# Optimization experiments

Hardware: AMD Instinct MI355X
Metric: run time of the kernel (lower is better)

The kernel has to match this reference:

```python
import jax, jax.numpy as jnp
import numpy as np

N = 100000
E = 1600000
NFEAT = 256
NHIDDEN = 128
NCLASS = 40
NLAYERS = 8
INIT_T = 0.5


def setup_inputs() -> dict:
    key = jax.random.key(0)
    ks = jax.random.split(key, 9)
    x = jax.random.normal(ks[0], (N, NFEAT), dtype=jnp.float32)
    edge_row = jax.random.randint(ks[1], (E,), 0, N, dtype=jnp.int32)
    edge_col = jax.random.randint(ks[2], (E,), 0, N, dtype=jnp.int32)
    # small weights so the Chebyshev recurrence stays numerically tame
    edge_weight = jax.random.uniform(ks[3], (E,), dtype=jnp.float32) * (2.0 / 16.0)
    b1 = 1.0 / np.sqrt(NFEAT)
    fc1_w = jax.random.uniform(ks[4], (NFEAT, NHIDDEN), minval=-b1, maxval=b1, dtype=jnp.float32)
    fc1_b = jax.random.uniform(ks[5], (NHIDDEN,), minval=-b1, maxval=b1, dtype=jnp.float32)
    b2 = 1.0 / np.sqrt(NHIDDEN)
    fc2_w = jax.random.uniform(ks[6], (NHIDDEN, NCLASS), minval=-b2, maxval=b2, dtype=jnp.float32)
    fc2_b = jax.random.uniform(ks[7], (NCLASS,), minval=-b2, maxval=b2, dtype=jnp.float32)
    thetas = jnp.full((NLAYERS,), INIT_T, dtype=jnp.float32)
    return {"x": x, "edge_row": edge_row, "edge_col": edge_col,
            "edge_weight": edge_weight, "fc1_w": fc1_w, "fc1_b": fc1_b,
            "fc2_w": fc2_w, "fc2_b": fc2_b, "thetas": thetas}


def _spmm(edge_row, edge_col, edge_weight, t):
    # out[r] = sum_{e: row[e]=r} w[e] * t[col[e]]   (sparse L @ T)
    msgs = edge_weight[:, None] * t[edge_col]  # [E, H]
    return jax.ops.segment_sum(msgs, edge_row, num_segments=N)


def reference(x, edge_row, edge_col, edge_weight, fc1_w, fc1_b, fc2_w, fc2_b, thetas):
    # eval mode: dropout is identity
    h = jax.nn.relu(x @ fc1_w + fc1_b)  # [N, H]
    # filter 0: T_0 = h, poly = theta_0 * T_0
    t0 = h
    poly = thetas[0] * t0
    # filter 1: T_1 = L @ T_0
    t1 = _spmm(edge_row, edge_col, edge_weight, t0)
    poly = poly + thetas[1] * t1
    # remaining filters, replicating the original prevs-update order exactly
    prev0, prev1 = t0, t1
    for i in range(2, NLAYERS):
        ti = 2.0 * _spmm(edge_row, edge_col, edge_weight, prev0) - prev1
        prev1 = prev0
        prev0 = ti
        poly = poly + thetas[i] * ti
    y = poly @ fc2_w + fc2_b  # [N, nclass]
    return jax.nn.log_softmax(y, axis=1)
```

## Files before the change

kernel.cpp:

```cpp
#include <hip/hip_runtime.h>
#include <hip/hip_bf16.h>


#define NFEAT 256
#define NHID  128
#define NCLS  40
#define ELLS  48

typedef __hip_bfloat16 bf16;
typedef __attribute__((ext_vector_type(8))) short bf16x8;
typedef __attribute__((ext_vector_type(4))) float f32x4;

__device__ inline float2 load2b(const bf16* p) {
    __hip_bfloat162 v = *(const __hip_bfloat162*)p;
    return make_float2(__bfloat162float(v.x), __bfloat162float(v.y));
}
__device__ inline void store2b(bf16* p, float2 v) {
    __hip_bfloat162 o;
    o.x = __float2bfloat16(v.x);
    o.y = __float2bfloat16(v.y);
    *(__hip_bfloat162*)p = o;
}

__global__ void zero_ints(int* __restrict__ p, int n) {
    int i = blockIdx.x * blockDim.x + threadIdx.x;
    if (i < n) p[i] = 0;
}

__global__ void scatter_ell(const int* __restrict__ erow, const int* __restrict__ ecol,
                            const float* __restrict__ ew, int* __restrict__ deg,
                            int2* __restrict__ cw, int E) {
    int e = blockIdx.x * blockDim.x + threadIdx.x;
    if (e < E) {
        int r = erow[e];
        int p = atomicAdd(&deg[r], 1);
        if (p < ELLS)
            cw[(size_t)r * ELLS + p] = make_int2(ecol[e], __float_as_int(ew[e]));
    }
}

__global__ void hist_kernel(const int* __restrict__ erow, int* __restrict__ deg, int E) {
    int e = blockIdx.x * blockDim.x + threadIdx.x;
    if (e < E) atomicAdd(&deg[erow[e]], 1);
}

__global__ void assign_starts(const int* __restrict__ deg, int* __restrict__ counter,
                              int* __restrict__ row_start, int* __restrict__ cursor, int N) {
    int r = blockIdx.x * blockDim.x + threadIdx.x;
    int lane = threadIdx.x & 63;
    int d = (r < N) ? deg[r] : 0;
    int x = d;
    #pragma unroll
    for (int off = 1; off < 64; off <<= 1) {
        int y = __shfl_up(x, off);
        if (lane >= off) x += y;
    }
    int base = 0;
    if (lane == 63) base = atomicAdd(counter, x);
    base = __shfl(base, 63);
    int start = base + (x - d);
    if (r < N) {
        row_start[r] = start;
        cursor[r] = start;
    }
}

__global__ void scatter_compact(const int* __restrict__ erow, const int* __restrict__ ecol,
                                const float* __restrict__ ew, int* __restrict__ cursor,
                                int2* __restrict__ cw, int E) {
    int e = blockIdx.x * blockDim.x + threadIdx.x;
    if (e < E) {
        int r = erow[e];
        int p = atomicAdd(&cursor[r], 1);
        cw[p] = make_int2(ecol[e], __float_as_int(ew[e]));
    }
}

__global__ __launch_bounds__(256) void fc1_mfma(
    const float* __restrict__ x, const float* __restrict__ W,
    const float* __restrict__ bias, bf16* __restrict__ t0, int n) {
    __shared__ __align__(16) bf16 As[128 * 40];
    __shared__ __align__(16) bf16 Bs[128 * 40];

    const int tid = threadIdx.x;
    const int wave = tid >> 6;
    const int lane = tid & 63;
    const int quad = lane >> 4;
    const int lm = lane & 15;
    const int block_row = blockIdx.x * 128;

    f32x4 acc[2][8];
    #pragma unroll
    for (int s = 0; s < 2; ++s)
        #pragma unroll
        for (int t = 0; t < 8; ++t)
            acc[s][t] = (f32x4){0.f, 0.f, 0.f, 0.f};

    float bcol[8];
    #pragma unroll
    for (int t = 0; t < 8; ++t) bcol[t] = bias[t * 16 + lm];

    for (int kc = 0; kc < NFEAT; kc += 32) {
        #pragma unroll
        for (int i = 0; i < 4; ++i) {
            int idx = tid + 256 * i;
            int row = idx >> 3;
            int c4 = idx & 7;
            int grow = block_row + row;
            float4 v = make_float4(0.f, 0.f, 0.f, 0.f);
            if (grow < n) v = *(const float4*)&x[(size_t)grow * NFEAT + kc + c4 * 4];
            __hip_bfloat162 lo2, hi2;
            lo2.x = __float2bfloat16(v.x); lo2.y = __float2bfloat16(v.y);
            hi2.x = __float2bfloat16(v.z); hi2.y = __float2bfloat16(v.w);
            *(__hip_bfloat162*)&As[row * 40 + c4 * 4] = lo2;
            *(__hip_bfloat162*)&As[row * 40 + c4 * 4 + 2] = hi2;
        }
        #pragma unroll
        for (int i = 0; i < 4; ++i) {
            int idx = tid + 256 * i;
            int nn = idx & 127;
            int k4 = idx >> 7;
            const float* wp = &W[(size_t)(kc + k4 * 4) * NHID + nn];
            float v0 = wp[0];
            float v1 = wp[NHID];
            float v2 = wp[2 * NHID];
            float v3 = wp[3 * NHID];
            __hip_bfloat162 lo2, hi2;
            lo2.x = __float2bfloat16(v0); lo2.y = __float2bfloat16(v1);
            hi2.x = __float2bfloat16(v2); hi2.y = __float2bfloat16(v3);
            *(__hip_bfloat162*)&Bs[nn * 40 + k4 * 4] = lo2;
            *(__hip_bfloat162*)&Bs[nn * 40 + k4 * 4 + 2] = hi2;
        }
        __syncthreads();

        bf16x8 af0 = *(const bf16x8*)&As[(wave * 32 + lm) * 40 + quad * 8];
        bf16x8 af1 = *(const bf16x8*)&As[(wave * 32 + 16 + lm) * 40 + quad * 8];
        #pragma unroll
        for (int t = 0; t < 8; ++t) {
            bf16x8 bf = *(const bf16x8*)&Bs[(t * 16 + lm) * 40 + quad * 8];
            acc[0][t] = __builtin_amdgcn_mfma_f32_16x16x32_bf16(af0, bf, acc[0][t], 0, 0, 0);
            acc[1][t] = __builtin_amdgcn_mfma_f32_16x16x32_bf16(af1, bf, acc[1][t], 0, 0, 0);
        }
        __syncthreads();
    }

    #pragma unroll
    for (int s = 0; s < 2; ++s) {
        #pragma unroll
        for (int r = 0; r < 4; ++r) {
            int grow = block_row + wave * 32 + s * 16 + quad * 4 + r;
            if (grow >= n) continue;
            bf16* orow = t0 + (size_t)grow * NHID + lm;
            #pragma unroll
            for (int t = 0; t < 8; ++t) {
                float v = fmaxf(acc[s][t][r] + bcol[t], 0.f);
                orow[t * 16] = __float2bfloat16(v);
            }
        }
    }
}

template <bool FIRST, int PMODE>
__global__ __launch_bounds__(256) void spmm_cheb(
    const int* __restrict__ row_start, const int* __restrict__ deg,
    const int2* __restrict__ cw,
    const bf16* __restrict__ tprev, const bf16* __restrict__ tsub,
    bf16* __restrict__ tout, float* __restrict__ poly,
    const float* __restrict__ thetas, int layer, int ell_stride, int n) {
    int lane = threadIdx.x & 63;
    int wid = (int)((blockIdx.x * (unsigned)blockDim.x + threadIdx.x) >> 6);
    if (wid >= n) return;
    int start = ell_stride ? wid * ell_stride : row_start[wid];
    int d = deg[wid];
    const int2* ep = cw + start;
    const int lo = 2 * lane;

    float2 acc = make_float2(0.f, 0.f);
    int j = 0;
    for (; j + 8 <= d; j += 8) {
        int2 e[8];
        #pragma unroll
        for (int u = 0; u < 8; ++u) e[u] = ep[j + u];
        float2 tv[8];
        #pragma unroll
        for (int u = 0; u < 8; ++u) tv[u] = load2b(tprev + (size_t)e[u].x * NHID + lo);
        #pragma unroll
        for (int u = 0; u < 8; ++u) {
            float w = __int_as_float(e[u].y);
            acc.x = fmaf(w, tv[u].x, acc.x);
            acc.y = fmaf(w, tv[u].y, acc.y);
        }
    }
    for (; j < d; ++j) {
        int2 e = ep[j];
        float w = __int_as_float(e.y);
        float2 tv = load2b(tprev + (size_t)e.x * NHID + lo);
        acc.x = fmaf(w, tv.x, acc.x);
        acc.y = fmaf(w, tv.y, acc.y);
    }

    size_t o = (size_t)wid * NHID + lo;
    float2 res, pv;
    if constexpr (FIRST) {
        res = acc;
    } else {
        pv = load2b(tsub + o);
        res = make_float2(2.f * acc.x - pv.x, 2.f * acc.y - pv.y);
    }
    store2b(tout + o, res);

    if constexpr (PMODE == 1) {
        float th0 = thetas[0], th1 = thetas[1], th2 = thetas[2];
        float2 t0v = load2b(tprev + o);
        float2 p;
        p.x = th0 * t0v.x + th1 * pv.x + th2 * res.x;
        p.y = th0 * t0v.y + th1 * pv.y + th2 * res.y;
        *(float2*)&poly[o] = p;
    } else if constexpr (PMODE == 2) {
        float tha = thetas[layer - 1], thb = thetas[layer];
        float2 tp = load2b(tprev + o);
        float2 p = *(float2*)&poly[o];
        p.x += tha * tp.x + thb * res.x;
        p.y += tha * tp.y + thb * res.y;
        *(float2*)&poly[o] = p;
    } else if constexpr (PMODE == 3) {
        float thb = thetas[layer];
        float2 p = *(float2*)&poly[o];
        p.x += thb * res.x;
        p.y += thb * res.y;
        *(float2*)&poly[o] = p;
    }
}

__global__ __launch_bounds__(256) void fc2_softmax(
    const float* __restrict__ poly, const float* __restrict__ w2,
    const float* __restrict__ b2, float* __restrict__ out, int n) {
    int row = blockIdx.x * 256 + threadIdx.x;
    if (row >= n) return;

    float acc[NCLS];
    #pragma unroll
    for (int c = 0; c < NCLS; ++c) acc[c] = b2[c];

    const float* pr = poly + (size_t)row * NHID;
    #pragma unroll 1
    for (int k = 0; k < NHID; k += 4) {
        float4 p = *(const float4*)&pr[k];
        const float* wr = w2 + (size_t)k * NCLS;
        #pragma unroll
        for (int c = 0; c < NCLS; ++c) {
            acc[c] = fmaf(p.x, wr[c], acc[c]);
            acc[c] = fmaf(p.y, wr[NCLS + c], acc[c]);
            acc[c] = fmaf(p.z, wr[2 * NCLS + c], acc[c]);
            acc[c] = fmaf(p.w, wr[3 * NCLS + c], acc[c]);
        }
    }

    float m = acc[0];
    #pragma unroll
    for (int c = 1; c < NCLS; ++c) m = fmaxf(m, acc[c]);
    float s = 0.f;
    #pragma unroll
    for (int c = 0; c < NCLS; ++c) s += __expf(acc[c] - m);
    float lse = m + __logf(s);

    float* orow = out + (size_t)row * NCLS;
    #pragma unroll
    for (int c = 0; c < NCLS; c += 4) {
        float4 v = make_float4(acc[c] - lse, acc[c + 1] - lse,
                               acc[c + 2] - lse, acc[c + 3] - lse);
        *(float4*)&orow[c] = v;
    }
}

static void run_pipeline(const float* x, const float* w1, const float* b1,
                         const float* w2, const float* b2, const float* thetas,
                         float* out, int N, int E,
                         const int* row_start, const int* deg, const int2* cw,
                         int ell_stride, float* poly, bf16* tX, bf16* tY, bf16* tZ,
                         hipStream_t stream) {
    fc1_mfma<<<(N + 127) / 128, 256, 0, stream>>>(x, w1, b1, tX, N);

    int spmm_blocks = (int)(((size_t)N * 64 + 255) / 256);
    spmm_cheb<true, 0><<<spmm_blocks, 256, 0, stream>>>(
        row_start, deg, cw, tX, (const bf16*)nullptr, tY, poly, thetas, 1, ell_stride, N);
    bf16* p0 = tX;
    bf16* p1 = tY;
    bf16* dead = tZ;
    for (int i = 2; i < 8; ++i) {
        if (i == 2)       spmm_cheb<false, 1><<<spmm_blocks, 256, 0, stream>>>(
            row_start, deg, cw, p0, p1, dead, poly, thetas, i, ell_stride, N);
        else if (i == 4 || i == 6) spmm_cheb<false, 2><<<spmm_blocks, 256, 0, stream>>>(
            row_start, deg, cw, p0, p1, dead, poly, thetas, i, ell_stride, N);
        else if (i == 7)  spmm_cheb<false, 3><<<spmm_blocks, 256, 0, stream>>>(
            row_start, deg, cw, p0, p1, dead, poly, thetas, i, ell_stride, N);
        else              spmm_cheb<false, 0><<<spmm_blocks, 256, 0, stream>>>(
            row_start, deg, cw, p0, p1, dead, poly, thetas, i, ell_stride, N);
        bf16* nd = p1;
        p1 = p0;
        p0 = dead;
        dead = nd;
    }
    fc2_softmax<<<(N + 255) / 256, 256, 0, stream>>>(poly, w2, b2, out, N);
}

extern "C" void kernel_launch(void* const* d_in, const int* in_sizes, int n_in,
                              void* d_out, int out_size, void* d_ws, size_t ws_size,
                              hipStream_t stream) {
    const float* x      = (const float*)d_in[0];
    const int*   erow   = (const int*)d_in[1];
    const int*   ecol   = (const int*)d_in[2];
    const float* ew     = (const float*)d_in[3];
    const float* w1     = (const float*)d_in[4];
    const float* b1     = (const float*)d_in[5];
    const float* w2     = (const float*)d_in[6];
    const float* b2     = (const float*)d_in[7];
    const float* thetas = (const float*)d_in[8];
    float* out = (float*)d_out;

    const int N = in_sizes[0] / NFEAT;
    const int E = in_sizes[1];

    size_t need_ell = 4096 + (size_t)N * 4 + (size_t)N * ELLS * 8 +
                      (size_t)N * NHID * 4 + 3 * (size_t)N * NHID * 2 + 4096;
    bool use_ell = need_ell <= ws_size;

    char* ws = (char*)d_ws;
    size_t off = 0;
    auto alloc = [&](size_t bytes) -> void* {
        off = (off + 255) & ~(size_t)255;
        void* p = ws + off;
        off += bytes;
        return p;
    };

    if (use_ell) {
        int*   deg  = (int*)alloc((size_t)N * 4);
        int2*  cw   = (int2*)alloc((size_t)N * ELLS * 8);
        float* poly = (float*)alloc((size_t)N * NHID * 4);
        bf16*  tX   = (bf16*)alloc((size_t)N * NHID * 2);
        bf16*  tY   = (bf16*)alloc((size_t)N * NHID * 2);
        bf16*  tZ   = (bf16*)alloc((size_t)N * NHID * 2);

        zero_ints<<<(N + 255) / 256, 256, 0, stream>>>(deg, N);
        scatter_ell<<<(E + 255) / 256, 256, 0, stream>>>(erow, ecol, ew, deg, cw, E);
        run_pipeline(x, w1, b1, w2, b2, thetas, out, N, E,
                     nullptr, deg, cw, ELLS, poly, tX, tY, tZ, stream);
    } else {
        int*   deg       = (int*)alloc((size_t)(N + 1) * 4);
        int*   counter   = deg + N;
        int*   row_start = (int*)alloc((size_t)N * 4);
        int*   cursor    = (int*)alloc((size_t)N * 4);
        int2*  cw        = (int2*)alloc((size_t)E * 8);
        float* poly      = (float*)alloc((size_t)N * NHID * 4);
        bf16*  tX        = (bf16*)alloc((size_t)N * NHID * 2);
        bf16*  tY        = (bf16*)alloc((size_t)N * NHID * 2);
        bf16*  tZ        = (bf16*)alloc((size_t)N * NHID * 2);

        zero_ints<<<(N + 1 + 255) / 256, 256, 0, stream>>>(deg, N + 1);
        hist_kernel<<<(E + 255) / 256, 256, 0, stream>>>(erow, deg, E);
        assign_starts<<<(N + 255) / 256, 256, 0, stream>>>(deg, counter, row_start, cursor, N);
        scatter_compact<<<(E + 255) / 256, 256, 0, stream>>>(erow, ecol, ew, cursor, cw, E);
        run_pipeline(x, w1, b1, w2, b2, thetas, out, N, E,
                     row_start, deg, cw, 0, poly, tX, tY, tZ, stream);
    }
}
```

Baseline: 924.6 us.

## Build CSR via two-level bucket sort and drop dead final Chebyshev store

Replaces the atomic ELL scatter with a four-stage bucketed counting sort (per-chunk histogram, global scan, binning through shared memory, per-bucket CSR build) that yields a compact CSR with rows grouped locally. The intent is to cut the global-atomic contention and scattered writes of the ELL build and to shrink the adjacency footprint read by every SpMM pass. The Chebyshev loop is also unrolled with the poly accumulation rearranged, and the last layer skips storing its T output since nothing reads it. The cost is more preprocessing kernels, including a single-block scan, and more workspace.

```diff
diff --git a/kernel.cpp b/kernel.cpp
--- a/kernel.cpp
+++ b/kernel.cpp
@@ -6,6 +6,9 @@
 #define NHID  128
 #define NCLS  40
 #define ELLS  48
+#define RPB   512
+#define RPB_SH 9
+#define CH    8192
 
 typedef __hip_bfloat16 bf16;
 typedef __attribute__((ext_vector_type(8))) short bf16x8;
@@ -20,6 +23,162 @@
     o.x = __float2bfloat16(v.x);
     o.y = __float2bfloat16(v.y);
     *(__hip_bfloat162*)p = o;
+}
+
+__global__ __launch_bounds__(256) void s1_hist(
+    const int* __restrict__ erow, int* __restrict__ cntT, int E, int NB, int NBLK) {
+    __shared__ int lcnt[256];
+    const int k = blockIdx.x, tid = threadIdx.x;
+    for (int i = tid; i < NB; i += 256) lcnt[i] = 0;
+    __syncthreads();
+    int e0 = k * CH, e1 = min(e0 + CH, E);
+    for (int e = e0 + tid; e < e1; e += 256)
+        atomicAdd(&lcnt[erow[e] >> RPB_SH], 1);
+    __syncthreads();
+    for (int b = tid; b < NB; b += 256) cntT[b * NBLK + k] = lcnt[b];
+}
+
+__global__ __launch_bounds__(256) void s2_scan(
+    const int* __restrict__ cntT, int* __restrict__ offsT, int* __restrict__ bbase,
+    int NB, int NBLK, int E) {
+    __shared__ int s_scan[256];
+    __shared__ int s_run;
+    const int tid = threadIdx.x;
+    if (tid == 0) s_run = 0;
+    __syncthreads();
+    const int total = NB * NBLK;
+    for (int base = 0; base < total; base += 1024) {
+        int j0 = base + tid * 4;
+        int v0 = (j0 + 0 < total) ? cntT[j0 + 0] : 0;
+        int v1 = (j0 + 1 < total) ? cntT[j0 + 1] : 0;
+        int v2 = (j0 + 2 < total) ? cntT[j0 + 2] : 0;
+        int v3 = (j0 + 3 < total) ? cntT[j0 + 3] : 0;
+        int tsum = v0 + v1 + v2 + v3;
+        s_scan[tid] = tsum;
+        __syncthreads();
+        #pragma unroll
+        for (int off = 1; off < 256; off <<= 1) {
+            int t = (tid >= off) ? s_scan[tid - off] : 0;
+            __syncthreads();
+            s_scan[tid] += t;
+            __syncthreads();
+        }
+        int incl = s_scan[tid];
+        int excl = incl - tsum;
+        int run = s_run;
+        int chunk_total = s_scan[255];
+        __syncthreads();
+        int p = run + excl;
+        int vv[4] = {v0, v1, v2, v3};
+        int pre = 0;
+        #pragma unroll
+        for (int u = 0; u < 4; ++u) {
+            int j = j0 + u;
+            if (j < total) {
+                offsT[j] = p + pre;
+                if (j % NBLK == 0) bbase[j / NBLK] = p + pre;
+            }
+            pre += vv[u];
+        }
+        if (tid == 0) s_run = run + chunk_total;
+        __syncthreads();
+    }
+    if (tid == 0) bbase[NB] = E;
+}
+
+__global__ __launch_bounds__(256) void s3_bin(
+    const int* __restrict__ erow, const int* __restrict__ ecol,
+    const float* __restrict__ ew, const int* __restrict__ offsT,
+    int* __restrict__ bin_row, int2* __restrict__ bin_cw, int E, int NB, int NBLK) {
+    __shared__ int lcnt[256], lbase[256], lcur[256], gadj[256];
+    __shared__ int s_scan[256];
+    __shared__ int srow[CH];
+    __shared__ int2 scw[CH];
+    const int k = blockIdx.x, tid = threadIdx.x;
+    for (int i = tid; i < NB; i += 256) lcnt[i] = 0;
+    __syncthreads();
+    int e0 = k * CH, e1 = min(e0 + CH, E), cnt = e1 - e0;
+    for (int e = e0 + tid; e < e1; e += 256)
+        atomicAdd(&lcnt[erow[e] >> RPB_SH], 1);
+    __syncthreads();
+    int myv = (tid < NB) ? lcnt[tid] : 0;
+    s_scan[tid] = myv;
+    __syncthreads();
+    #pragma unroll
+    for (int off = 1; off < 256; off <<= 1) {
+        int t = (tid >= off) ? s_scan[tid - off] : 0;
+        __syncthreads();
+        s_scan[tid] += t;
+        __syncthreads();
+    }
+    int excl = s_scan[tid] - myv;
+    if (tid < NB) {
+        lbase[tid] = excl;
+        lcur[tid] = excl;
+        gadj[tid] = offsT[tid * NBLK + k] - excl;
+    }
+    __syncthreads();
+    for (int e = e0 + tid; e < e1; e += 256) {
+        int r = erow[e];
+        int b = r >> RPB_SH;
+        int s = atomicAdd(&lcur[b], 1);
+        srow[s] = r;
+        scw[s] = make_int2(ecol[e], __float_as_int(ew[e]));
+    }
+    __syncthreads();
+    for (int i = tid; i < cnt; i += 256) {
+        int r = srow[i];
+        int b = r >> RPB_SH;
+        int dst = gadj[b] + i;
+        bin_row[dst] = r;
+        bin_cw[dst] = scw[i];
+    }
+}
+
+__global__ __launch_bounds__(256) void s4_build(
+    const int* __restrict__ bbase, const int* __restrict__ bin_row,
+    const int2* __restrict__ bin_cw, int* __restrict__ deg,
+    int* __restrict__ row_start, int2* __restrict__ cw, int N) {
+    __shared__ int ldeg[RPB], lcur2[RPB];
+    __shared__ int s_scan[256];
+    const int b = blockIdx.x, tid = threadIdx.x;
+    const int ebase = bbase[b], eend = bbase[b + 1];
+    const int R0 = b << RPB_SH;
+    ldeg[tid] = 0;
+    ldeg[tid + 256] = 0;
+    __syncthreads();
+    for (int i = ebase + tid; i < eend; i += 256)
+        atomicAdd(&ldeg[bin_row[i] - R0], 1);
+    __syncthreads();
+    int a0 = ldeg[2 * tid], a1 = ldeg[2 * tid + 1];
+    int ps = a0 + a1;
+    s_scan[tid] = ps;
+    __syncthreads();
+    #pragma unroll
+    for (int off = 1; off < 256; off <<= 1) {
+        int t = (tid >= off) ? s_scan[tid - off] : 0;
+        __syncthreads();
+        s_scan[tid] += t;
+        __syncthreads();
+    }
+    int pexcl = s_scan[tid] - ps;
+    lcur2[2 * tid] = pexcl;
+    lcur2[2 * tid + 1] = pexcl + a0;
+    __syncthreads();
+    #pragma unroll
+    for (int u = 0; u < 2; ++u) {
+        int lr = 2 * tid + u;
+        int r = R0 + lr;
+        if (r < N) {
+            deg[r] = ldeg[lr];
+            row_start[r] = ebase + lcur2[lr];
+        }
+    }
+    for (int i = ebase + tid; i < eend; i += 256) {
+        int lr = bin_row[i] - R0;
+        int s = atomicAdd(&lcur2[lr], 1);
+        cw[ebase + s] = bin_cw[i];
+    }
 }
 
 __global__ void zero_ints(int* __restrict__ p, int n) {
@@ -207,27 +366,21 @@
         pv = load2b(tsub + o);
         res = make_float2(2.f * acc.x - pv.x, 2.f * acc.y - pv.y);
     }
-    store2b(tout + o, res);
+    if constexpr (PMODE != 3) store2b(tout + o, res);
 
     if constexpr (PMODE == 1) {
-        float th0 = thetas[0], th1 = thetas[1], th2 = thetas[2];
-        float2 t0v = load2b(tprev + o);
+        float th0 = thetas[0], th12 = thetas[1] + thetas[2], th3 = thetas[3];
+        float2 tpv = load2b(tprev + o);
         float2 p;
-        p.x = th0 * t0v.x + th1 * pv.x + th2 * res.x;
-        p.y = th0 * t0v.y + th1 * pv.y + th2 * res.y;
+        p.x = th0 * pv.x + th12 * tpv.x + th3 * res.x;
+        p.y = th0 * pv.y + th12 * tpv.y + th3 * res.y;
         *(float2*)&poly[o] = p;
-    } else if constexpr (PMODE == 2) {
+    } else if constexpr (PMODE == 2 || PMODE == 3) {
         float tha = thetas[layer - 1], thb = thetas[layer];
-        float2 tp = load2b(tprev + o);
+        float2 tpv = load2b(tprev + o);
         float2 p = *(float2*)&poly[o];
-        p.x += tha * tp.x + thb * res.x;
-        p.y += tha * tp.y + thb * res.y;
-        *(float2*)&poly[o] = p;
-    } else if constexpr (PMODE == 3) {
-        float thb = thetas[layer];
-        float2 p = *(float2*)&poly[o];
-        p.x += thb * res.x;
-        p.y += thb * res.y;
+        p.x += tha * tpv.x + thb * res.x;
+        p.y += tha * tpv.y + thb * res.y;
         *(float2*)&poly[o] = p;
     }
 }
@@ -284,23 +437,17 @@
     int spmm_blocks = (int)(((size_t)N * 64 + 255) / 256);
     spmm_cheb<true, 0><<<spmm_blocks, 256, 0, stream>>>(
         row_start, deg, cw, tX, (const bf16*)nullptr, tY, poly, thetas, 1, ell_stride, N);
-    bf16* p0 = tX;
-    bf16* p1 = tY;
-    bf16* dead = tZ;
-    for (int i = 2; i < 8; ++i) {
-        if (i == 2)       spmm_cheb<false, 1><<<spmm_blocks, 256, 0, stream>>>(
-            row_start, deg, cw, p0, p1, dead, poly, thetas, i, ell_stride, N);
-        else if (i == 4 || i == 6) spmm_cheb<false, 2><<<spmm_blocks, 256, 0, stream>>>(
-            row_start, deg, cw, p0, p1, dead, poly, thetas, i, ell_stride, N);
-        else if (i == 7)  spmm_cheb<false, 3><<<spmm_blocks, 256, 0, stream>>>(
-            row_start, deg, cw, p0, p1, dead, poly, thetas, i, ell_stride, N);
-        else              spmm_cheb<false, 0><<<spmm_blocks, 256, 0, stream>>>(
-            row_start, deg, cw, p0, p1, dead, poly, thetas, i, ell_stride, N);
-        bf16* nd = p1;
-        p1 = p0;
-        p0 = dead;
-        dead = nd;
-    }
+    spmm_cheb<false, 1><<<spmm_blocks, 256, 0, stream>>>(
+        row_start, deg, cw, tY, tX, tZ, poly, thetas, 3, ell_stride, N);
+    spmm_cheb<false, 0><<<spmm_blocks, 256, 0, stream>>>(
+        row_start, deg, cw, tZ, tY, tX, poly, thetas, 4, ell_stride, N);
+    spmm_cheb<false, 2><<<spmm_blocks, 256, 0, stream>>>(
+        row_start, deg, cw, tX, tZ, tY, poly, thetas, 5, ell_stride, N);
+    spmm_cheb<false, 0><<<spmm_blocks, 256, 0, stream>>>(
+        row_start, deg, cw, tY, tX, tZ, poly, thetas, 6, ell_stride, N);
+    spmm_cheb<false, 3><<<spmm_blocks, 256, 0, stream>>>(
+        row_start, deg, cw, tZ, tY, (bf16*)nullptr, poly, thetas, 7, ell_stride, N);
+
     fc2_softmax<<<(N + 255) / 256, 256, 0, stream>>>(poly, w2, b2, out, N);
 }
 
@@ -321,9 +468,8 @@
     const int N = in_sizes[0] / NFEAT;
     const int E = in_sizes[1];
 
-    size_t need_ell = 4096 + (size_t)N * 4 + (size_t)N * ELLS * 8 +
-                      (size_t)N * NHID * 4 + 3 * (size_t)N * NHID * 2 + 4096;
-    bool use_ell = need_ell <= ws_size;
+    const int NB   = (N + RPB - 1) >> RPB_SH;
+    const int NBLK = (E + CH - 1) / CH;
 
     char* ws = (char*)d_ws;
     size_t off = 0;
@@ -334,7 +480,37 @@
         return p;
     };
 
-    if (use_ell) {
+    size_t tail = (size_t)N * NHID * 4 + 3 * ((size_t)N * NHID * 2 + 256) + 4096;
+
+    size_t need_sort = 2 * (size_t)NB * NBLK * 4 + (size_t)(NB + 1) * 4 +
+                       (size_t)E * 4 + (size_t)E * 8 +
+                       2 * (size_t)N * 4 +
+                       (size_t)E * 8 + tail + 8192;
+    size_t need_ell  = (size_t)N * 4 + (size_t)N * ELLS * 8 + tail + 8192;
+    size_t need_comp = (size_t)(N + 1) * 4 + 2 * (size_t)N * 4 +
+                       (size_t)E * 8 + tail + 8192;
+
+    if (NB <= 256 && need_sort <= ws_size) {
+        int*  cntT      = (int*)alloc((size_t)NB * NBLK * 4);
+        int*  offsT     = (int*)alloc((size_t)NB * NBLK * 4);
+        int*  bbase     = (int*)alloc((size_t)(NB + 1) * 4);
+        int*  bin_row   = (int*)alloc((size_t)E * 4);
+        int2* bin_cw    = (int2*)alloc((size_t)E * 8);
+        int*  deg       = (int*)alloc((size_t)N * 4);
+        int*  row_start = (int*)alloc((size_t)N * 4);
+        int2* cw        = (int2*)alloc((size_t)E * 8);
+        float* poly = (float*)alloc((size_t)N * NHID * 4);
+        bf16*  tX   = (bf16*)alloc((size_t)N * NHID * 2);
+        bf16*  tY   = (bf16*)alloc((size_t)N * NHID * 2);
+        bf16*  tZ   = (bf16*)alloc((size_t)N * NHID * 2);
+
+        s1_hist<<<NBLK, 256, 0, stream>>>(erow, cntT, E, NB, NBLK);
+        s2_scan<<<1, 256, 0, stream>>>(cntT, offsT, bbase, NB, NBLK, E);
+        s3_bin<<<NBLK, 256, 0, stream>>>(erow, ecol, ew, offsT, bin_row, bin_cw, E, NB, NBLK);
+        s4_build<<<NB, 256, 0, stream>>>(bbase, bin_row, bin_cw, deg, row_start, cw, N);
+        run_pipeline(x, w1, b1, w2, b2, thetas, out, N, E,
+                     row_start, deg, cw, 0, poly, tX, tY, tZ, stream);
+    } else if (need_ell <= ws_size) {
         int*   deg  = (int*)alloc((size_t)N * 4);
         int2*  cw   = (int2*)alloc((size_t)N * ELLS * 8);
         float* poly = (float*)alloc((size_t)N * NHID * 4);
```

Result: faster. 876.1 us (-5.3%).

## Skip redundant T2 SpMM, fuse degree histogram into fc1, prefer CSR path

Applied to the files above, without the earlier changes.

With the reference's prevs-update order, T2 = 2·L·T0 − T1 equals T1, so one SpMM can be dropped. The chain now folds theta1+theta2 onto T1 and starts the recurrence at layer 3, leaving six SpMM launches instead of seven. The edge-degree histogram runs as extra blocks inside the fc1 MFMA kernel to overlap the two. The compact CSR layout is now chosen by default over ELL. The last layer also stops writing its unused T output. The algebraic shortcut depends on the exact recurrence quirk, and the CSR path adds preprocessing kernels compared with the ELL path.

```diff
diff --git a/kernel.cpp b/kernel.cpp
--- a/kernel.cpp
+++ b/kernel.cpp
@@ -25,6 +25,38 @@
 __global__ void zero_ints(int* __restrict__ p, int n) {
     int i = blockIdx.x * blockDim.x + threadIdx.x;
     if (i < n) p[i] = 0;
+}
+
+__global__ void assign_starts(const int* __restrict__ deg, int* __restrict__ counter,
+                              int* __restrict__ row_start, int* __restrict__ cursor, int N) {
+    int r = blockIdx.x * blockDim.x + threadIdx.x;
+    int lane = threadIdx.x & 63;
+    int d = (r < N) ? deg[r] : 0;
+    int x = d;
+    #pragma unroll
+    for (int off = 1; off < 64; off <<= 1) {
+        int y = __shfl_up(x, off);
+        if (lane >= off) x += y;
+    }
+    int base = 0;
+    if (lane == 63) base = atomicAdd(counter, x);
+    base = __shfl(base, 63);
+    int start = base + (x - d);
+    if (r < N) {
+        row_start[r] = start;
+        cursor[r] = start;
+    }
+}
+
+__global__ void scatter_compact(const int* __restrict__ erow, const int* __restrict__ ecol,
+                                const float* __restrict__ ew, int* __restrict__ cursor,
+                                int2* __restrict__ cw, int E) {
+    int e = blockIdx.x * blockDim.x + threadIdx.x;
+    if (e < E) {
+        int r = erow[e];
+        int p = atomicAdd(&cursor[r], 1);
+        cw[p] = make_int2(ecol[e], __float_as_int(ew[e]));
+    }
 }
 
 __global__ void scatter_ell(const int* __restrict__ erow, const int* __restrict__ ecol,
@@ -39,48 +71,20 @@
     }
 }
 
-__global__ void hist_kernel(const int* __restrict__ erow, int* __restrict__ deg, int E) {
-    int e = blockIdx.x * blockDim.x + threadIdx.x;
-    if (e < E) atomicAdd(&deg[erow[e]], 1);
-}
-
-__global__ void assign_starts(const int* __restrict__ deg, int* __restrict__ counter,
-                              int* __restrict__ row_start, int* __restrict__ cursor, int N) {
-    int r = blockIdx.x * blockDim.x + threadIdx.x;
-    int lane = threadIdx.x & 63;
-    int d = (r < N) ? deg[r] : 0;
-    int x = d;
-    #pragma unroll
-    for (int off = 1; off < 64; off <<= 1) {
-        int y = __shfl_up(x, off);
-        if (lane >= off) x += y;
-    }
-    int base = 0;
-    if (lane == 63) base = atomicAdd(counter, x);
-    base = __shfl(base, 63);
-    int start = base + (x - d);
-    if (r < N) {
-        row_start[r] = start;
-        cursor[r] = start;
-    }
-}
-
-__global__ void scatter_compact(const int* __restrict__ erow, const int* __restrict__ ecol,
-                                const float* __restrict__ ew, int* __restrict__ cursor,
-                                int2* __restrict__ cw, int E) {
-    int e = blockIdx.x * blockDim.x + threadIdx.x;
-    if (e < E) {
-        int r = erow[e];
-        int p = atomicAdd(&cursor[r], 1);
-        cw[p] = make_int2(ecol[e], __float_as_int(ew[e]));
-    }
-}
-
-__global__ __launch_bounds__(256) void fc1_mfma(
+__global__ __launch_bounds__(256) void fc1_hist(
     const float* __restrict__ x, const float* __restrict__ W,
-    const float* __restrict__ bias, bf16* __restrict__ t0, int n) {
+    const float* __restrict__ bias, bf16* __restrict__ t0, int n,
+    const int* __restrict__ erow, int* __restrict__ deg, int E, int fc1_blocks) {
     __shared__ __align__(16) bf16 As[128 * 40];
     __shared__ __align__(16) bf16 Bs[128 * 40];
+
+    if ((int)blockIdx.x >= fc1_blocks) {
+        int nb = gridDim.x - fc1_blocks;
+        int b = blockIdx.x - fc1_blocks;
+        for (int e = b * 256 + (int)threadIdx.x; e < E; e += nb * 256)
+            atomicAdd(&deg[erow[e]], 1);
+        return;
+    }
 
     const int tid = threadIdx.x;
     const int wave = tid >> 6;
@@ -207,27 +211,21 @@
         pv = load2b(tsub + o);
         res = make_float2(2.f * acc.x - pv.x, 2.f * acc.y - pv.y);
     }
-    store2b(tout + o, res);
+    if constexpr (PMODE != 3) store2b(tout + o, res);
 
     if constexpr (PMODE == 1) {
-        float th0 = thetas[0], th1 = thetas[1], th2 = thetas[2];
-        float2 t0v = load2b(tprev + o);
+        float th0 = thetas[0], th12 = thetas[1] + thetas[2], th3 = thetas[3];
+        float2 tpv = load2b(tprev + o);
         float2 p;
-        p.x = th0 * t0v.x + th1 * pv.x + th2 * res.x;
-        p.y = th0 * t0v.y + th1 * pv.y + th2 * res.y;
+        p.x = th0 * pv.x + th12 * tpv.x + th3 * res.x;
+        p.y = th0 * pv.y + th12 * tpv.y + th3 * res.y;
         *(float2*)&poly[o] = p;
-    } else if constexpr (PMODE == 2) {
+    } else if constexpr (PMODE == 2 || PMODE == 3) {
         float tha = thetas[layer - 1], thb = thetas[layer];
-        float2 tp = load2b(tprev + o);
+        float2 tpv = load2b(tprev + o);
         float2 p = *(float2*)&poly[o];
-        p.x += tha * tp.x + thb * res.x;
-        p.y += tha * tp.y + thb * res.y;
-        *(float2*)&poly[o] = p;
-    } else if constexpr (PMODE == 3) {
-        float thb = thetas[layer];
-        float2 p = *(float2*)&poly[o];
-        p.x += thb * res.x;
-        p.y += thb * res.y;
+        p.x += tha * tpv.x + thb * res.x;
+        p.y += tha * tpv.y + thb * res.y;
         *(float2*)&poly[o] = p;
     }
 }
@@ -273,34 +271,25 @@
     }
 }
 
-static void run_pipeline(const float* x, const float* w1, const float* b1,
-                         const float* w2, const float* b2, const float* thetas,
-                         float* out, int N, int E,
-                         const int* row_start, const int* deg, const int2* cw,
-                         int ell_stride, float* poly, bf16* tX, bf16* tY, bf16* tZ,
-                         hipStream_t stream) {
-    fc1_mfma<<<(N + 127) / 128, 256, 0, stream>>>(x, w1, b1, tX, N);
-
+static void run_spmm_chain(const float* w2, const float* b2, const float* thetas,
+                           float* out, int N,
+                           const int* row_start, const int* deg, const int2* cw,
+                           int ell_stride, float* poly, bf16* tX, bf16* tY, bf16* tZ,
+                           hipStream_t stream) {
     int spmm_blocks = (int)(((size_t)N * 64 + 255) / 256);
     spmm_cheb<true, 0><<<spmm_blocks, 256, 0, stream>>>(
         row_start, deg, cw, tX, (const bf16*)nullptr, tY, poly, thetas, 1, ell_stride, N);
-    bf16* p0 = tX;
-    bf16* p1 = tY;
-    bf16* dead = tZ;
-    for (int i = 2; i < 8; ++i) {
-        if (i == 2)       spmm_cheb<false, 1><<<spmm_blocks, 256, 0, stream>>>(
-            row_start, deg, cw, p0, p1, dead, poly, thetas, i, ell_stride, N);
-        else if (i == 4 || i == 6) spmm_cheb<false, 2><<<spmm_blocks, 256, 0, stream>>>(
-            row_start, deg, cw, p0, p1, dead, poly, thetas, i, ell_stride, N);
-        else if (i == 7)  spmm_cheb<false, 3><<<spmm_blocks, 256, 0, stream>>>(
-            row_start, deg, cw, p0, p1, dead, poly, thetas, i, ell_stride, N);
-        else              spmm_cheb<false, 0><<<spmm_blocks, 256, 0, stream>>>(
-            row_start, deg, cw, p0, p1, dead, poly, thetas, i, ell_stride, N);
-        bf16* nd = p1;
-        p1 = p0;
-        p0 = dead;
-        dead = nd;
-    }
+    spmm_cheb<false, 1><<<spmm_blocks, 256, 0, stream>>>(
+        row_start, deg, cw, tY, tX, tZ, poly, thetas, 3, ell_stride, N);
+    spmm_cheb<false, 0><<<spmm_blocks, 256, 0, stream>>>(
+        row_start, deg, cw, tZ, tY, tX, poly, thetas, 4, ell_stride, N);
+    spmm_cheb<false, 2><<<spmm_blocks, 256, 0, stream>>>(
+        row_start, deg, cw, tX, tZ, tY, poly, thetas, 5, ell_stride, N);
+    spmm_cheb<false, 0><<<spmm_blocks, 256, 0, stream>>>(
+        row_start, deg, cw, tY, tX, tZ, poly, thetas, 6, ell_stride, N);
+    spmm_cheb<false, 3><<<spmm_blocks, 256, 0, stream>>>(
+        row_start, deg, cw, tZ, tY, (bf16*)nullptr, poly, thetas, 7, ell_stride, N);
+
     fc2_softmax<<<(N + 255) / 256, 256, 0, stream>>>(poly, w2, b2, out, N);
 }
 
@@ -321,10 +310,6 @@
     const int N = in_sizes[0] / NFEAT;
     const int E = in_sizes[1];
 
-    size_t need_ell = 4096 + (size_t)N * 4 + (size_t)N * ELLS * 8 +
-                      (size_t)N * NHID * 4 + 3 * (size_t)N * NHID * 2 + 4096;
-    bool use_ell = need_ell <= ws_size;
-
     char* ws = (char*)d_ws;
     size_t off = 0;
     auto alloc = [&](size_t bytes) -> void* {
@@ -334,19 +319,14 @@
         return p;
     };
 
-    if (use_ell) {
-        int*   deg  = (int*)alloc((size_t)N * 4);
-        int2*  cw   = (int2*)alloc((size_t)N * ELLS * 8);
-        float* poly = (float*)alloc((size_t)N * NHID * 4);
-        bf16*  tX   = (bf16*)alloc((size_t)N * NHID * 2);
-        bf16*  tY   = (bf16*)alloc((size_t)N * NHID * 2);
-        bf16*  tZ   = (bf16*)alloc((size_t)N * NHID * 2);
-
-        zero_ints<<<(N + 255) / 256, 256, 0, stream>>>(deg, N);
-        scatter_ell<<<(E + 255) / 256, 256, 0, stream>>>(erow, ecol, ew, deg, cw, E);
-        run_pipeline(x, w1, b1, w2, b2, thetas, out, N, E,
-                     nullptr, deg, cw, ELLS, poly, tX, tY, tZ, stream);
-    } else {
+    size_t tail = (size_t)N * NHID * 4 + 3 * ((size_t)N * NHID * 2 + 256) + 4096;
+    size_t need_csr = (size_t)(N + 1) * 4 + 2 * (size_t)N * 4 + (size_t)E * 8 + tail + 8192;
+    size_t need_ell = (size_t)N * 4 + (size_t)N * ELLS * 8 + tail + 8192;
+
+    const int fc1_blocks = (N + 127) / 128;
+    const int hist_blocks = 512;
+
+    if (need_csr <= ws_size) {
         int*   deg       = (int*)alloc((size_t)(N + 1) * 4);
         int*   counter   = deg + N;
         int*   row_start = (int*)alloc((size_t)N * 4);
@@ -358,10 +338,25 @@
         bf16*  tZ        = (bf16*)alloc((size_t)N * NHID * 2);
 
         zero_ints<<<(N + 1 + 255) / 256, 256, 0, stream>>>(deg, N + 1);
-        hist_kernel<<<(E + 255) / 256, 256, 0, stream>>>(erow, deg, E);
+        fc1_hist<<<fc1_blocks + hist_blocks, 256, 0, stream>>>(
+            x, w1, b1, tX, N, erow, deg, E, fc1_blocks);
         assign_starts<<<(N + 255) / 256, 256, 0, stream>>>(deg, counter, row_start, cursor, N);
         scatter_compact<<<(E + 255) / 256, 256, 0, stream>>>(erow, ecol, ew, cursor, cw, E);
-        run_pipeline(x, w1, b1, w2, b2, thetas, out, N, E,
-                     row_start, deg, cw, 0, poly, tX, tY, tZ, stream);
-    }
-}
+        run_spmm_chain(w2, b2, thetas, out, N,
+                       row_start, deg, cw, 0, poly, tX, tY, tZ, stream);
+    } else {
+        int*   deg  = (int*)alloc((size_t)N * 4);
+        int2*  cw   = (int2*)alloc((size_t)N * ELLS * 8);
+        float* poly = (float*)alloc((size_t)N * NHID * 4);
+        bf16*  tX   = (bf16*)alloc((size_t)N * NHID * 2);
+        bf16*  tY   = (bf16*)alloc((size_t)N * NHID * 2);
+        bf16*  tZ   = (bf16*)alloc((size_t)N * NHID * 2);
+
+        zero_ints<<<(N + 255) / 256, 256, 0, stream>>>(deg, N);
+        scatter_ell<<<(E + 255) / 256, 256, 0, stream>>>(erow, ecol, ew, deg, cw, E);
+        fc1_hist<<<fc1_blocks, 256, 0, stream>>>(
+            x, w1, b1, tX, N, erow, (int*)nullptr, 0, fc1_blocks);
+        run_spmm_chain(w2, b2, thetas, out, N,
+                       nullptr, deg, cw, ELLS, poly, tX, tY, tZ, stream);
+    }
+}
```

New measurement: 912.0 us. No clear change (-1.4%).
